# Kernel optimization log

Measured on AMD Instinct MI355X. Metric: run time of the kernel, lower is better.

The kernel has to match this reference:

```python
import jax, jax.numpy as jnp
import numpy as np

N, H, E = 50000, 128, 1600000

def setup_inputs() -> dict:
    key = jax.random.key(0)
    k1, k2, k3, k4 = jax.random.split(key, 4)
    h = jax.random.normal(k1, (N, H), dtype=jnp.float32)
    edge_index = jax.random.randint(k2, (2, E), 0, N, dtype=jnp.int64)
    # edge_scorer: Linear(2H, 1); node_scorer: Linear(H, 1)
    W_edge = jax.random.normal(k3, (2 * H, 1), dtype=jnp.float32) / np.sqrt(2 * H)
    b_edge = jnp.zeros((1,), dtype=jnp.float32)
    W_node = jax.random.normal(k4, (H, 1), dtype=jnp.float32) / np.sqrt(H)
    b_node = jnp.zeros((1,), dtype=jnp.float32)
    return {"h": h, "edge_index": edge_index, "W_edge": W_edge,
            "b_edge": b_edge, "W_node": W_node, "b_node": b_node}

def reference(h, edge_index, W_edge, b_edge, W_node, b_node):
    n = h.shape[0]
    src, dst = edge_index[0], edge_index[1]
    # cat([h[src], h[dst]]) @ W_edge == (h @ W_src)[src] + (h @ W_dst)[dst]
    # (same math as the torch module, avoids materializing the (E, 2H) concat)
    W_src, W_dst = W_edge[:h.shape[1]], W_edge[h.shape[1]:]
    s_src = (h @ W_src)[:, 0]            # (N,)
    s_dst = (h @ W_dst)[:, 0]            # (N,)
    edge_scores = s_src[src] + s_dst[dst] + b_edge[0]   # (E,)
    node_edge_score = jax.ops.segment_sum(edge_scores, dst, num_segments=n)
    node_self_score = (h @ W_node)[:, 0] + b_node[0]    # (N,)
    combined = node_edge_score + node_self_score
    return jax.nn.softmax(combined, axis=0)
```

## Files before the change

### kernel.cpp

```cpp
#include <hip/hip_runtime.h>
#include <math.h>


#define RANGE_BITS 14
#define RANGE_SIZE (1 << RANGE_BITS)

__device__ __forceinline__ void atomicMaxFloat(float* addr, float val) {
    if (val >= 0.0f) atomicMax((int*)addr, __float_as_int(val));
    else             atomicMin((unsigned int*)addr, __float_as_uint(val));
}

__global__ __launch_bounds__(256) void node_scores_kernel(
    const float* __restrict__ h,
    const float* __restrict__ W_edge,
    const float* __restrict__ b_edge,
    const float* __restrict__ W_node,
    const float* __restrict__ b_node,
    float* __restrict__ s_src,
    float* __restrict__ t_dst,
    float* __restrict__ self_sc,
    float* __restrict__ acc,
    float* __restrict__ gmax,
    float* __restrict__ gsum,
    int N, int H)
{
    if (blockIdx.x == 0 && threadIdx.x == 0) { *gmax = -INFINITY; *gsum = 0.0f; }

    const int lane16 = threadIdx.x & 15;
    const int n = (blockIdx.x * blockDim.x + threadIdx.x) >> 4;
    if (n >= N) return;

    const float4* __restrict__ h4  = (const float4*)(h + (size_t)n * H);
    const float4* __restrict__ ws4 = (const float4*)(W_edge);
    const float4* __restrict__ wd4 = (const float4*)(W_edge + H);
    const float4* __restrict__ wn4 = (const float4*)(W_node);
    const int H4 = H >> 2;

    float ps = 0.0f, pd = 0.0f, pn = 0.0f;
    for (int i = lane16; i < H4; i += 16) {
        float4 hv = h4[i];
        float4 a = ws4[i], b = wd4[i], c = wn4[i];
        ps = fmaf(hv.x, a.x, fmaf(hv.y, a.y, fmaf(hv.z, a.z, fmaf(hv.w, a.w, ps))));
        pd = fmaf(hv.x, b.x, fmaf(hv.y, b.y, fmaf(hv.z, b.z, fmaf(hv.w, b.w, pd))));
        pn = fmaf(hv.x, c.x, fmaf(hv.y, c.y, fmaf(hv.z, c.z, fmaf(hv.w, c.w, pn))));
    }
    #pragma unroll
    for (int off = 8; off > 0; off >>= 1) {
        ps += __shfl_xor(ps, off, 64);
        pd += __shfl_xor(pd, off, 64);
        pn += __shfl_xor(pn, off, 64);
    }
    if (lane16 == 0) {
        float self = pn + b_node[0];
        s_src[n]   = ps;
        t_dst[n]   = pd + b_edge[0];
        self_sc[n] = self;
        acc[n]     = self;
    }
}

__global__ __launch_bounds__(512) void edge_bin_kernel(
    const int* __restrict__ ei,
    const float* __restrict__ s_src,
    const float* __restrict__ t_dst,
    float* __restrict__ partials,
    int N, int E, int chunk, int vec_ok)
{
    __shared__ float hist[RANGE_SIZE];
    const int b  = blockIdx.x;
    const int r  = blockIdx.y;
    const int lo = r << RANGE_BITS;
    const int hi = min(lo + RANGE_SIZE, N);

    for (int i = threadIdx.x; i < RANGE_SIZE; i += blockDim.x) hist[i] = 0.0f;
    __syncthreads();

    const int e0 = b * chunk;
    const int e1 = min(e0 + chunk, E);
    if (e0 < e1) {
        if (vec_ok) {
            const int nvec = (e1 - e0) >> 2;
            const int4* __restrict__ src4 = (const int4*)(ei + e0);
            const int4* __restrict__ dst4 = (const int4*)(ei + E + e0);
            for (int i = threadIdx.x; i < nvec; i += blockDim.x) {
                int4 d = dst4[i];
                int4 s = src4[i];
                if (d.x >= lo && d.x < hi) atomicAdd(&hist[d.x - lo], s_src[s.x] + t_dst[d.x]);
                if (d.y >= lo && d.y < hi) atomicAdd(&hist[d.y - lo], s_src[s.y] + t_dst[d.y]);
                if (d.z >= lo && d.z < hi) atomicAdd(&hist[d.z - lo], s_src[s.z] + t_dst[d.z]);
                if (d.w >= lo && d.w < hi) atomicAdd(&hist[d.w - lo], s_src[s.w] + t_dst[d.w]);
            }
            for (int e = e0 + 4 * nvec + threadIdx.x; e < e1; e += blockDim.x) {
                int d = ei[E + e];
                if (d >= lo && d < hi) atomicAdd(&hist[d - lo], s_src[ei[e]] + t_dst[d]);
            }
        } else {
            for (int e = e0 + threadIdx.x; e < e1; e += blockDim.x) {
                int d = ei[E + e];
                if (d >= lo && d < hi) atomicAdd(&hist[d - lo], s_src[ei[e]] + t_dst[d]);
            }
        }
    }
    __syncthreads();

    float* __restrict__ outp = partials + (size_t)b * N + lo;
    const int len = hi - lo;
    for (int i = threadIdx.x; i < len; i += blockDim.x) outp[i] = hist[i];
}

__global__ __launch_bounds__(256) void edge_accum_fallback_kernel(
    const int* __restrict__ ei,
    const float* __restrict__ s_src,
    const float* __restrict__ t_dst,
    float* __restrict__ acc,
    int E)
{
    int e = blockIdx.x * blockDim.x + threadIdx.x;
    if (e >= E) return;
    int s = ei[e];
    int d = ei[E + e];
    atomicAdd(&acc[d], s_src[s] + t_dst[d]);
}

__global__ __launch_bounds__(256) void combine_max_kernel(
    const float* __restrict__ self_sc,
    const float* __restrict__ partials,
    float* __restrict__ acc,
    float* __restrict__ gmax,
    int N, int B, int use_partials)
{
    float m = -INFINITY;
    for (int i = blockIdx.x * blockDim.x + threadIdx.x; i < N;
         i += gridDim.x * blockDim.x) {
        float v;
        if (use_partials) {
            float v0 = self_sc[i], v1 = 0.0f, v2 = 0.0f, v3 = 0.0f;
            int b = 0;
            for (; b + 4 <= B; b += 4) {
                v0 += partials[(size_t)(b + 0) * N + i];
                v1 += partials[(size_t)(b + 1) * N + i];
                v2 += partials[(size_t)(b + 2) * N + i];
                v3 += partials[(size_t)(b + 3) * N + i];
            }
            for (; b < B; ++b) v0 += partials[(size_t)b * N + i];
            v = (v0 + v1) + (v2 + v3);
            acc[i] = v;
        } else {
            v = acc[i];
        }
        m = fmaxf(m, v);
    }
    #pragma unroll
    for (int off = 32; off > 0; off >>= 1)
        m = fmaxf(m, __shfl_xor(m, off, 64));
    __shared__ float smax[4];
    int wave = threadIdx.x >> 6, lane = threadIdx.x & 63;
    if (lane == 0) smax[wave] = m;
    __syncthreads();
    if (threadIdx.x == 0) {
        float bm = smax[0];
        for (int w = 1; w < (int)(blockDim.x >> 6); ++w) bm = fmaxf(bm, smax[w]);
        atomicMaxFloat(gmax, bm);
    }
}

__global__ __launch_bounds__(256) void exp_sum_kernel(
    const float* __restrict__ acc, const float* __restrict__ gmax,
    float* __restrict__ out, float* __restrict__ gsum, int N)
{
    const float mx = *gmax;
    float s = 0.0f;
    for (int i = blockIdx.x * blockDim.x + threadIdx.x; i < N;
         i += gridDim.x * blockDim.x) {
        float v = __expf(acc[i] - mx);
        out[i] = v;
        s += v;
    }
    #pragma unroll
    for (int off = 32; off > 0; off >>= 1)
        s += __shfl_xor(s, off, 64);
    __shared__ float ssum[4];
    int wave = threadIdx.x >> 6, lane = threadIdx.x & 63;
    if (lane == 0) ssum[wave] = s;
    __syncthreads();
    if (threadIdx.x == 0) {
        float bs = 0.0f;
        for (int w = 0; w < (int)(blockDim.x >> 6); ++w) bs += ssum[w];
        atomicAdd(gsum, bs);
    }
}

__global__ __launch_bounds__(256) void normalize_kernel(
    float* __restrict__ out, const float* __restrict__ gsum, int N)
{
    int i = blockIdx.x * blockDim.x + threadIdx.x;
    if (i >= N) return;
    out[i] *= (1.0f / *gsum);
}

extern "C" void kernel_launch(void* const* d_in, const int* in_sizes, int n_in,
                              void* d_out, int out_size, void* d_ws, size_t ws_size,
                              hipStream_t stream) {
    const float* h      = (const float*)d_in[0];
    const int*   ei     = (const int*)  d_in[1];
    const float* W_edge = (const float*)d_in[2];
    const float* b_edge = (const float*)d_in[3];
    const float* W_node = (const float*)d_in[4];
    const float* b_node = (const float*)d_in[5];

    const int H = in_sizes[2] / 2;
    const int N = in_sizes[0] / H;
    const int E = in_sizes[1] / 2;

    float* out    = (float*)d_out;
    float* ws     = (float*)d_ws;
    float* s_src  = ws;
    float* t_dst  = ws + (size_t)N;
    float* self_s = ws + 2 * (size_t)N;
    float* acc    = ws + 3 * (size_t)N;
    float* gmax   = ws + 4 * (size_t)N;
    float* gsum   = ws + 4 * (size_t)N + 1;
    float* partials = ws + 4 * (size_t)N + 2;

    const size_t base_floats = 4 * (size_t)N + 2;
    int B = 0;
    if (ws_size / sizeof(float) > base_floats) {
        size_t avail = ws_size / sizeof(float) - base_floats;
        B = (int)(avail / (size_t)N);
    }
    if (B > 64) B = 64;
    const int R = (N + RANGE_SIZE - 1) >> RANGE_BITS;
    const int use_partials = (B >= 16) ? 1 : 0;

    {
        int threads = N * 16;
        int grid = (threads + 255) / 256;
        node_scores_kernel<<<grid, 256, 0, stream>>>(
            h, W_edge, b_edge, W_node, b_node,
            s_src, t_dst, self_s, acc, gmax, gsum, N, H);
    }
    if (use_partials) {
        int chunk = (((E + B - 1) / B) + 3) & ~3;
        int vec_ok = ((E & 3) == 0) ? 1 : 0;
        dim3 grid(B, R);
        edge_bin_kernel<<<grid, 512, 0, stream>>>(
            ei, s_src, t_dst, partials, N, E, chunk, vec_ok);
    } else {
        int grid = (E + 255) / 256;
        edge_accum_fallback_kernel<<<grid, 256, 0, stream>>>(ei, s_src, t_dst, acc, E);
    }
    combine_max_kernel<<<256, 256, 0, stream>>>(self_s, partials, acc, gmax, N, B, use_partials);
    {
        int grid = (N + 255) / 256;
        exp_sum_kernel<<<grid, 256, 0, stream>>>(acc, gmax, out, gsum, N);
    }
    {
        int grid = (N + 255) / 256;
        normalize_kernel<<<grid, 256, 0, stream>>>(out, gsum, N);
    }
}
```

Before: 119.4 us.

## Fuse softmax finalize into one cooperative kernel and widen edge binning blocks

The three finalize kernels (combine+max, exp+sum, normalize) are replaced by a single cooperative kernel. It keeps each thread's values in registers and uses grid.sync for the global max and sum, which removes two launches and the re-reads of acc and out. The edge binning kernel now runs 1024-thread blocks, loads source indices as scalars only when the destination falls in range, and writes its histogram back with float4 stores. The cooperative launch needs device support and enough co-resident blocks, and the per-thread item limit caps N.

Result: slower. 186.4 us (+56.1%).

```diff
diff --git a/kernel.cpp b/kernel.cpp
--- a/kernel.cpp
+++ b/kernel.cpp
@@ -1,9 +1,16 @@
 #include <hip/hip_runtime.h>
+#include <hip/hip_cooperative_groups.h>
 #include <math.h>
+
+namespace cg = cooperative_groups;
 
 
 #define RANGE_BITS 14
 #define RANGE_SIZE (1 << RANGE_BITS)
+#define NCHUNKS 64
+#define COOP_BLOCKS 256
+#define COOP_THREADS 256
+#define MAXITEMS 4
 
 __device__ __forceinline__ void atomicMaxFloat(float* addr, float val) {
     if (val >= 0.0f) atomicMax((int*)addr, __float_as_int(val));
@@ -59,7 +66,7 @@
     }
 }
 
-__global__ __launch_bounds__(512) void edge_bin_kernel(
+__global__ __launch_bounds__(1024) void edge_bin_kernel(
     const int* __restrict__ ei,
     const float* __restrict__ s_src,
     const float* __restrict__ t_dst,
@@ -80,15 +87,14 @@
     if (e0 < e1) {
         if (vec_ok) {
             const int nvec = (e1 - e0) >> 2;
-            const int4* __restrict__ src4 = (const int4*)(ei + e0);
             const int4* __restrict__ dst4 = (const int4*)(ei + E + e0);
             for (int i = threadIdx.x; i < nvec; i += blockDim.x) {
                 int4 d = dst4[i];
-                int4 s = src4[i];
-                if (d.x >= lo && d.x < hi) atomicAdd(&hist[d.x - lo], s_src[s.x] + t_dst[d.x]);
-                if (d.y >= lo && d.y < hi) atomicAdd(&hist[d.y - lo], s_src[s.y] + t_dst[d.y]);
-                if (d.z >= lo && d.z < hi) atomicAdd(&hist[d.z - lo], s_src[s.z] + t_dst[d.z]);
-                if (d.w >= lo && d.w < hi) atomicAdd(&hist[d.w - lo], s_src[s.w] + t_dst[d.w]);
+                const int eb = e0 + 4 * i;
+                if (d.x >= lo && d.x < hi) atomicAdd(&hist[d.x - lo], s_src[ei[eb + 0]] + t_dst[d.x]);
+                if (d.y >= lo && d.y < hi) atomicAdd(&hist[d.y - lo], s_src[ei[eb + 1]] + t_dst[d.y]);
+                if (d.z >= lo && d.z < hi) atomicAdd(&hist[d.z - lo], s_src[ei[eb + 2]] + t_dst[d.z]);
+                if (d.w >= lo && d.w < hi) atomicAdd(&hist[d.w - lo], s_src[ei[eb + 3]] + t_dst[d.w]);
             }
             for (int e = e0 + 4 * nvec + threadIdx.x; e < e1; e += blockDim.x) {
                 int d = ei[E + e];
@@ -105,7 +111,14 @@
 
     float* __restrict__ outp = partials + (size_t)b * N + lo;
     const int len = hi - lo;
-    for (int i = threadIdx.x; i < len; i += blockDim.x) outp[i] = hist[i];
+    if (((len & 3) == 0)) {
+        const int len4 = len >> 2;
+        const float4* __restrict__ h4 = (const float4*)hist;
+        float4* __restrict__ o4 = (float4*)outp;
+        for (int i = threadIdx.x; i < len4; i += blockDim.x) o4[i] = h4[i];
+    } else {
+        for (int i = threadIdx.x; i < len; i += blockDim.x) outp[i] = hist[i];
+    }
 }
 
 __global__ __launch_bounds__(256) void edge_accum_fallback_kernel(
@@ -120,6 +133,105 @@
     int s = ei[e];
     int d = ei[E + e];
     atomicAdd(&acc[d], s_src[s] + t_dst[d]);
+}
+
+__device__ __forceinline__ float blockReduceMaxB(float v) {
+    __shared__ float sm[16];
+    #pragma unroll
+    for (int off = 32; off > 0; off >>= 1) v = fmaxf(v, __shfl_xor(v, off, 64));
+    const int w = threadIdx.x >> 6, l = threadIdx.x & 63;
+    const int nw = blockDim.x >> 6;
+    if (l == 0) sm[w] = v;
+    __syncthreads();
+    float r = sm[0];
+    for (int i = 1; i < nw; ++i) r = fmaxf(r, sm[i]);
+    __syncthreads();
+    return r;
+}
+
+__device__ __forceinline__ float blockReduceSumB(float v) {
+    __shared__ float sm[16];
+    #pragma unroll
+    for (int off = 32; off > 0; off >>= 1) v += __shfl_xor(v, off, 64);
+    const int w = threadIdx.x >> 6, l = threadIdx.x & 63;
+    const int nw = blockDim.x >> 6;
+    if (l == 0) sm[w] = v;
+    __syncthreads();
+    float r = 0.0f;
+    for (int i = 0; i < nw; ++i) r += sm[i];
+    __syncthreads();
+    return r;
+}
+
+__global__ __launch_bounds__(COOP_THREADS) void finalize_coop_kernel(
+    const float* __restrict__ self_sc,
+    const float* __restrict__ partials,
+    const float* __restrict__ acc,
+    float* __restrict__ out,
+    float* __restrict__ red,
+    int N, int B, int use_partials)
+{
+    cg::grid_group grid = cg::this_grid();
+    const int gid   = blockIdx.x * blockDim.x + threadIdx.x;
+    const int gsize = gridDim.x * blockDim.x;
+
+    float vals[MAXITEMS];
+    float m = -INFINITY;
+    #pragma unroll
+    for (int k = 0; k < MAXITEMS; ++k) {
+        const int i = gid + k * gsize;
+        if (i < N) {
+            float v;
+            if (use_partials) {
+                float v0 = self_sc[i], v1 = 0.0f, v2 = 0.0f, v3 = 0.0f;
+                int b = 0;
+                for (; b + 4 <= B; b += 4) {
+                    v0 += partials[(size_t)(b + 0) * N + i];
+                    v1 += partials[(size_t)(b + 1) * N + i];
+                    v2 += partials[(size_t)(b + 2) * N + i];
+                    v3 += partials[(size_t)(b + 3) * N + i];
+                }
+                for (; b < B; ++b) v0 += partials[(size_t)b * N + i];
+                v = (v0 + v1) + (v2 + v3);
+            } else {
+                v = acc[i];
+            }
+            vals[k] = v;
+            m = fmaxf(m, v);
+        } else {
+            vals[k] = -INFINITY;
+        }
+    }
+
+    m = blockReduceMaxB(m);
+    if (threadIdx.x == 0) red[blockIdx.x] = m;
+    grid.sync();
+
+    float t = (threadIdx.x < gridDim.x) ? red[threadIdx.x] : -INFINITY;
+    const float gmaxv = blockReduceMaxB(t);
+
+    float s = 0.0f;
+    #pragma unroll
+    for (int k = 0; k < MAXITEMS; ++k) {
+        const int i = gid + k * gsize;
+        if (i < N) {
+            float e = __expf(vals[k] - gmaxv);
+            vals[k] = e;
+            s += e;
+        }
+    }
+    s = blockReduceSumB(s);
+    if (threadIdx.x == 0) red[gridDim.x + blockIdx.x] = s;
+    grid.sync();
+
+    float ts = (threadIdx.x < gridDim.x) ? red[gridDim.x + threadIdx.x] : 0.0f;
+    const float gsumv = blockReduceSumB(ts);
+    const float inv = 1.0f / gsumv;
+    #pragma unroll
+    for (int k = 0; k < MAXITEMS; ++k) {
+        const int i = gid + k * gsize;
+        if (i < N) out[i] = vals[k] * inv;
+    }
 }
 
 __global__ __launch_bounds__(256) void combine_max_kernel(
@@ -150,18 +262,8 @@
         }
         m = fmaxf(m, v);
     }
-    #pragma unroll
-    for (int off = 32; off > 0; off >>= 1)
-        m = fmaxf(m, __shfl_xor(m, off, 64));
-    __shared__ float smax[4];
-    int wave = threadIdx.x >> 6, lane = threadIdx.x & 63;
-    if (lane == 0) smax[wave] = m;
-    __syncthreads();
-    if (threadIdx.x == 0) {
-        float bm = smax[0];
-        for (int w = 1; w < (int)(blockDim.x >> 6); ++w) bm = fmaxf(bm, smax[w]);
-        atomicMaxFloat(gmax, bm);
-    }
+    m = blockReduceMaxB(m);
+    if (threadIdx.x == 0) atomicMaxFloat(gmax, m);
 }
 
 __global__ __launch_bounds__(256) void exp_sum_kernel(
@@ -176,18 +278,8 @@
         out[i] = v;
         s += v;
     }
-    #pragma unroll
-    for (int off = 32; off > 0; off >>= 1)
-        s += __shfl_xor(s, off, 64);
-    __shared__ float ssum[4];
-    int wave = threadIdx.x >> 6, lane = threadIdx.x & 63;
-    if (lane == 0) ssum[wave] = s;
-    __syncthreads();
-    if (threadIdx.x == 0) {
-        float bs = 0.0f;
-        for (int w = 0; w < (int)(blockDim.x >> 6); ++w) bs += ssum[w];
-        atomicAdd(gsum, bs);
-    }
+    s = blockReduceSumB(s);
+    if (threadIdx.x == 0) atomicAdd(gsum, s);
 }
 
 __global__ __launch_bounds__(256) void normalize_kernel(
@@ -212,25 +304,32 @@
     const int N = in_sizes[0] / H;
     const int E = in_sizes[1] / 2;
 
-    float* out    = (float*)d_out;
-    float* ws     = (float*)d_ws;
-    float* s_src  = ws;
-    float* t_dst  = ws + (size_t)N;
-    float* self_s = ws + 2 * (size_t)N;
-    float* acc    = ws + 3 * (size_t)N;
-    float* gmax   = ws + 4 * (size_t)N;
-    float* gsum   = ws + 4 * (size_t)N + 1;
-    float* partials = ws + 4 * (size_t)N + 2;
-
-    const size_t base_floats = 4 * (size_t)N + 2;
+    float* out     = (float*)d_out;
+    float* ws      = (float*)d_ws;
+    float* s_src   = ws;
+    float* t_dst   = ws + (size_t)N;
+    float* self_s  = ws + 2 * (size_t)N;
+    float* acc     = ws + 3 * (size_t)N;
+    float* gmax    = ws + 4 * (size_t)N;
+    float* gsum    = ws + 4 * (size_t)N + 1;
+    float* red     = ws + 4 * (size_t)N + 2;
+    float* partials = red + 2 * COOP_BLOCKS;
+
+    const size_t base_floats = 4 * (size_t)N + 2 + 2 * COOP_BLOCKS;
     int B = 0;
     if (ws_size / sizeof(float) > base_floats) {
         size_t avail = ws_size / sizeof(float) - base_floats;
         B = (int)(avail / (size_t)N);
     }
-    if (B > 64) B = 64;
+    if (B > NCHUNKS) B = NCHUNKS;
     const int R = (N + RANGE_SIZE - 1) >> RANGE_BITS;
     const int use_partials = (B >= 16) ? 1 : 0;
+
+    int dev = 0, coop = 0;
+    hipGetDevice(&dev);
+    hipDeviceGetAttribute(&coop, hipDeviceAttributeCooperativeLaunch, dev);
+    const int use_coop =
+        (coop && (size_t)N <= (size_t)COOP_BLOCKS * COOP_THREADS * MAXITEMS) ? 1 : 0;
 
     {
         int threads = N * 16;
@@ -243,19 +342,24 @@
         int chunk = (((E + B - 1) / B) + 3) & ~3;
         int vec_ok = ((E & 3) == 0) ? 1 : 0;
         dim3 grid(B, R);
-        edge_bin_kernel<<<grid, 512, 0, stream>>>(
+        edge_bin_kernel<<<grid, 1024, 0, stream>>>(
             ei, s_src, t_dst, partials, N, E, chunk, vec_ok);
     } else {
         int grid = (E + 255) / 256;
         edge_accum_fallback_kernel<<<grid, 256, 0, stream>>>(ei, s_src, t_dst, acc, E);
     }
-    combine_max_kernel<<<256, 256, 0, stream>>>(self_s, partials, acc, gmax, N, B, use_partials);
-    {
+    if (use_coop) {
+        void* args[] = { (void*)&self_s, (void*)&partials, (void*)&acc,
+                         (void*)&out, (void*)&red, (void*)&N, (void*)&B,
+                         (void*)&use_partials };
+        hipLaunchCooperativeKernel((void*)finalize_coop_kernel,
+                                   dim3(COOP_BLOCKS), dim3(COOP_THREADS),
+                                   args, 0, stream);
+    } else {
+        combine_max_kernel<<<256, 256, 0, stream>>>(
+            self_s, partials, acc, gmax, N, B, use_partials);
         int grid = (N + 255) / 256;
         exp_sum_kernel<<<grid, 256, 0, stream>>>(acc, gmax, out, gsum, N);
-    }
-    {
-        int grid = (N + 255) / 256;
         normalize_kernel<<<grid, 256, 0, stream>>>(out, gsum, N);
     }
 }
```
